# Kernel optimization log

Measured on AMD Instinct MI355X. Metric: run time of the kernel, lower is better.

Reference implementation:

```python
import jax, jax.numpy as jnp
import numpy as np

EMBED_DIM = 1024
HEAD_DIM = 64


def setup_inputs() -> dict:
    key = jax.random.key(0)
    ks = jax.random.split(key, 7)
    B, S = 4, 2048
    x = jax.random.normal(ks[0], (B, S, EMBED_DIM), dtype=jnp.float32)
    s = EMBED_DIM ** -0.5  # torch Linear default init scale (uniform bound)
    Wk = jax.random.uniform(ks[1], (EMBED_DIM, HEAD_DIM), minval=-s, maxval=s)
    bk = jax.random.uniform(ks[2], (HEAD_DIM,), minval=-s, maxval=s)
    Wq = jax.random.uniform(ks[3], (EMBED_DIM, HEAD_DIM), minval=-s, maxval=s)
    bq = jax.random.uniform(ks[4], (HEAD_DIM,), minval=-s, maxval=s)
    Wv = jax.random.uniform(ks[5], (EMBED_DIM, HEAD_DIM), minval=-s, maxval=s)
    bv = jax.random.uniform(ks[6], (HEAD_DIM,), minval=-s, maxval=s)
    return {"x": x, "Wq": Wq, "bq": bq, "Wk": Wk, "bk": bk, "Wv": Wv, "bv": bv}


def reference(x, Wq, bq, Wk, bk, Wv, bv):
    # projections: [B,S,D]
    q = x @ Wq + bq
    k = x @ Wk + bk
    v = x @ Wv + bv
    # NOTE: faithful to source, which DIVIDES by head_dim**-0.5 (i.e. multiplies by sqrt(d))
    scale = HEAD_DIM ** -0.5
    wei = jnp.einsum('bqd,bkd->bqk', q, k) / scale  # [B,S,S]
    S = x.shape[1]
    causal = jnp.tril(jnp.ones((S, S), dtype=bool))
    wei = jnp.where(causal, wei, -jnp.inf)
    attn_weights = jax.nn.softmax(wei, axis=-1)
    return jnp.einsum('bqk,bkd->bqd', attn_weights, v)
```

## Files before the change

kernel.cpp:

```cpp
#include <hip/hip_runtime.h>
#include <math.h>

#define S_LEN 2048
#define NB 4
#define EMB 1024
#define HD 64
#define NROW (NB * S_LEN)
#define NEG_BIG -3.0e38f
#define SC 11.5415603f
#define DEFER_THR 3.0f
#define KVSPLIT 4

typedef _Float16 half8 __attribute__((ext_vector_type(8)));
typedef _Float16 half4 __attribute__((ext_vector_type(4)));
typedef float f32x4 __attribute__((ext_vector_type(4)));

static __device__ __forceinline__ f32x4 mfma32(half8 a, half8 b, f32x4 c) {
    return __builtin_amdgcn_mfma_f32_16x16x32_f16(a, b, c, 0, 0, 0);
}
static __device__ __forceinline__ f32x4 mfma16(half4 a, half4 b, f32x4 c) {
    return __builtin_amdgcn_mfma_f32_16x16x16f16(a, b, c, 0, 0, 0);
}

__global__ __launch_bounds__(256) void prep_w(
    const float* __restrict__ Wq, const float* __restrict__ Wk,
    const float* __restrict__ Wv, _Float16* __restrict__ wt_frag)
{
    const int g  = blockIdx.x >> 4;
    const int kc = blockIdx.x & 15;
    const int k0 = kc * 64;
    const float* W = (g == 0) ? Wq : (g == 1) ? Wk : Wv;

    __shared__ float tile[64][68];
    const int t = threadIdx.x;
    {
        const int kk = t >> 2, cb = (t & 3) * 16;
#pragma unroll
        for (int i = 0; i < 4; i++)
            *(f32x4*)&tile[kk][cb + 4 * i] =
                *(const f32x4*)(W + (size_t)(k0 + kk) * HD + cb + 4 * i);
    }
    __syncthreads();

    const int c4 = t >> 6, l = t & 63;
    const int col = c4 * 16 + (l & 15);
    const int krow = (l >> 4) * 8;
#pragma unroll
    for (int sub = 0; sub < 2; sub++) {
        half8 hv;
#pragma unroll
        for (int e = 0; e < 8; e++)
            hv[e] = (_Float16)tile[sub * 32 + krow + e][col];
        const size_t addr = (size_t)(g * 4 + c4) * 16384 +
                            (size_t)(kc * 2 + sub) * 512 + (size_t)l * 8;
        *(half8*)(wt_frag + addr) = hv;
    }
}

__global__ __launch_bounds__(768) void proj_kernel(
    const float* __restrict__ x, const _Float16* __restrict__ wt_frag,
    const float* __restrict__ bq, const float* __restrict__ bk,
    const float* __restrict__ bv,
    _Float16* __restrict__ qs, _Float16* __restrict__ kh_,
    _Float16* __restrict__ vt)
{
    const int m0 = blockIdx.x * 32;
    const int t = threadIdx.x, lane = t & 63, w = t >> 6;

    __shared__ __align__(16) _Float16 xs[32][1032];

    for (int i = t; i < 4096; i += 768) {
        const int row = i >> 7, off = (i & 127) * 8;
        const float* xp = x + (size_t)(m0 + row) * EMB + off;
        const f32x4 v0 = *(const f32x4*)xp;
        const f32x4 v1 = *(const f32x4*)(xp + 4);
        half8 h;
#pragma unroll
        for (int jj = 0; jj < 4; jj++) {
            h[jj]     = (_Float16)v0[jj];
            h[4 + jj] = (_Float16)v1[jj];
        }
        *(half8*)&xs[row][off] = h;
    }

    const int f = w;
    const int row0 = lane & 15, kq = lane >> 4;
    const _Float16* wp = wt_frag + (size_t)f * 16384 + (size_t)lane * 8;

    half8 wbuf[4];
#pragma unroll
    for (int c = 0; c < 4; c++) wbuf[c] = *(const half8*)(wp + (size_t)c * 512);

    __syncthreads();

    f32x4 acc0 = f32x4{0, 0, 0, 0}, acc1 = f32x4{0, 0, 0, 0};

#pragma unroll
    for (int c = 0; c < 32; ++c) {
        const half8 ax0 = *(const half8*)&xs[row0][c * 32 + kq * 8];
        const half8 ax1 = *(const half8*)&xs[16 + row0][c * 32 + kq * 8];
        const half8 bw = wbuf[c & 3];
        acc0 = mfma32(ax0, bw, acc0);
        acc1 = mfma32(ax1, bw, acc1);
        if (c + 4 < 32) wbuf[c & 3] = *(const half8*)(wp + (size_t)(c + 4) * 512);
    }

    const int mat = f >> 2, c4 = f & 3;
    const int mcol = c4 * 16 + (lane & 15);
    const float bb = ((mat == 0) ? bq : (mat == 1) ? bk : bv)[mcol];
#pragma unroll
    for (int rh = 0; rh < 2; rh++) {
        const f32x4 acc = rh ? acc1 : acc0;
        const int grow0 = m0 + rh * 16 + kq * 4;
        if (mat == 0) {
#pragma unroll
            for (int r = 0; r < 4; r++)
                qs[(size_t)(grow0 + r) * HD + mcol] = (_Float16)((acc[r] + bb) * SC);
        } else if (mat == 1) {
#pragma unroll
            for (int r = 0; r < 4; r++)
                kh_[(size_t)(grow0 + r) * HD + mcol] = (_Float16)(acc[r] + bb);
        } else {
            half4 hv;
#pragma unroll
            for (int r = 0; r < 4; r++) hv[r] = (_Float16)(acc[r] + bb);
            const int bidx = grow0 >> 11, sr = grow0 & (S_LEN - 1);
            *(half4*)(vt + ((size_t)bidx * HD + mcol) * S_LEN + sr) = hv;
        }
    }
}

__global__ __launch_bounds__(512) void attn_kernel(
    const _Float16* __restrict__ qs, const _Float16* __restrict__ kh_,
    const _Float16* __restrict__ vt,
    _Float16* __restrict__ po, float* __restrict__ pm, float* __restrict__ pl)
{
    const int id = blockIdx.x;
    const int qq = id & 3;
    const int b  = (id >> 2) & 3;
    const int qt = 31 - (id >> 4);
    const int q0 = qt * 64;
    const int t = threadIdx.x, lane = t & 63, w = t >> 6;
    const int rf = w >> 1, kvh = w & 1;

    __shared__ __align__(16) unsigned char smem[37888];
    _Float16 (*klds)[64][72] = (_Float16(*)[64][72])smem;
    _Float16 (*vlds)[64][72] = (_Float16(*)[64][72])(smem + 18432);
    float (*obuf)[16][68] = (float(*)[16][68])smem;
    float* mbuf = (float*)(smem + 36864);
    float* lbuf = (float*)(smem + 36864 + 512);

    const size_t rowq = ((size_t)b * S_LEN + q0 + rf * 16 + (lane & 15)) * HD + (lane >> 4) * 8;
    const half8 bq0 = *(const half8*)(qs + rowq);
    const half8 bq1 = *(const half8*)(qs + rowq + 32);

    f32x4 o[4];
#pragma unroll
    for (int c = 0; c < 4; c++) o[c] = f32x4{0, 0, 0, 0};
    float m_r = NEG_BIG, l_r = 0.f;

    const int nt = qt + 1;
    const int lo = (nt * qq) >> 2, hi = (nt * (qq + 1)) >> 2;

    const size_t kbase = (size_t)b * S_LEN * HD;
    const size_t vbase = (size_t)b * HD * S_LEN;
    const int srow = t >> 3, scol = (t & 7) * 8;

    half8 sK, sV;
    auto gload = [&](int tl) {
        sK = *(const half8*)(kh_ + kbase + (size_t)(tl * 64 + srow) * HD + scol);
        sV = *(const half8*)(vt + vbase + (size_t)srow * S_LEN + tl * 64 + scol);
    };
    auto swrite = [&](int nb) {
        *(half8*)&klds[nb][srow][scol] = sK;
        *(half8*)&vlds[nb][srow][scol] = sV;
    };

    if (lo < hi) { gload(lo); swrite(0); }
    __syncthreads();

    int cur = 0;
    for (int tl = lo; tl < hi; ++tl) {
        if (tl + 1 < hi) gload(tl + 1);

        const int kv0 = tl * 64 + kvh * 32;
        __builtin_amdgcn_s_setprio(1);
        f32x4 s[2];
#pragma unroll
        for (int h = 0; h < 2; h++) {
            const int keyl = kvh * 32 + 16 * h + (lane & 15);
            f32x4 a = f32x4{0, 0, 0, 0};
            a = mfma32(*(const half8*)&klds[cur][keyl][(lane >> 4) * 8], bq0, a);
            a = mfma32(*(const half8*)&klds[cur][keyl][32 + (lane >> 4) * 8], bq1, a);
            s[h] = a;
        }
        __builtin_amdgcn_s_setprio(0);

        const int qrow = q0 + rf * 16 + (lane & 15);
        const int kb0  = kv0 + (lane >> 4) * 4;
        float tv[8];
#pragma unroll
        for (int h = 0; h < 2; h++)
#pragma unroll
            for (int r = 0; r < 4; r++)
                tv[h * 4 + r] = (kb0 + 16 * h + r <= qrow) ? s[h][r] : NEG_BIG;

        float mt = tv[0];
#pragma unroll
        for (int i = 1; i < 8; i++) mt = fmaxf(mt, tv[i]);
        mt = fmaxf(mt, __shfl_xor(mt, 16));
        mt = fmaxf(mt, __shfl_xor(mt, 32));

        if (!__all(mt <= m_r + DEFER_THR)) {
            const float mn = fmaxf(m_r, mt);
            const float corr = exp2f(m_r - mn);
            m_r = mn;
            l_r *= corr;
            float corrB[4];
#pragma unroll
            for (int r = 0; r < 4; r++) corrB[r] = __shfl(corr, (lane >> 4) * 4 + r);
#pragma unroll
            for (int c = 0; c < 4; c++)
#pragma unroll
                for (int r = 0; r < 4; r++) o[c][r] *= corrB[r];
        }

        float p[8], rs = 0.f;
#pragma unroll
        for (int i = 0; i < 8; i++) { p[i] = exp2f(tv[i] - m_r); rs += p[i]; }
        rs += __shfl_xor(rs, 16);
        rs += __shfl_xor(rs, 32);
        l_r += rs;

        half4 pa[2];
#pragma unroll
        for (int h = 0; h < 2; h++)
#pragma unroll
            for (int r = 0; r < 4; r++) pa[h][r] = (_Float16)p[h * 4 + r];
        __builtin_amdgcn_s_setprio(1);
#pragma unroll
        for (int c = 0; c < 4; c++) {
#pragma unroll
            for (int h = 0; h < 2; h++) {
                const half4 vf = *(const half4*)&vlds[cur][16 * c + (lane & 15)]
                                                    [kvh * 32 + 16 * h + (lane >> 4) * 4];
                o[c] = mfma16(pa[h], vf, o[c]);
            }
        }
        __builtin_amdgcn_s_setprio(0);

        if (tl + 1 < hi) swrite(cur ^ 1);
        __syncthreads();
        cur ^= 1;
    }

    if (lane < 16) { mbuf[w * 16 + lane] = m_r; lbuf[w * 16 + lane] = l_r; }
#pragma unroll
    for (int c = 0; c < 4; c++)
#pragma unroll
        for (int r = 0; r < 4; r++)
            obuf[w][(lane >> 4) * 4 + r][16 * c + (lane & 15)] = o[c][r];
    __syncthreads();

    if (t < 256) {
        const int row16 = t >> 4, cb = (t & 15) * 4;
#pragma unroll
        for (int rf2 = 0; rf2 < 4; rf2++) {
            const int w0 = rf2 * 2, w1 = w0 + 1;
            const float m0v = mbuf[w0 * 16 + row16], m1v = mbuf[w1 * 16 + row16];
            const float M = fmaxf(m0v, m1v);
            const float e0 = exp2f(m0v - M), e1 = exp2f(m1v - M);
            const float L = lbuf[w0 * 16 + row16] * e0 + lbuf[w1 * 16 + row16] * e1;
            const f32x4 o0 = *(const f32x4*)&obuf[w0][row16][cb];
            const f32x4 o1 = *(const f32x4*)&obuf[w1][row16][cb];
            half4 hv;
#pragma unroll
            for (int jj = 0; jj < 4; jj++) hv[jj] = (_Float16)(o0[jj] * e0 + o1[jj] * e1);
            const size_t idx = (size_t)(qq * NB + b) * S_LEN + q0 + rf2 * 16 + row16;
            *(half4*)(po + idx * HD + cb) = hv;
            if ((t & 15) == 0) { pm[idx] = M; pl[idx] = L; }
        }
    }
}

__global__ __launch_bounds__(256) void merge_kernel(
    const _Float16* __restrict__ po, const float* __restrict__ pm,
    const float* __restrict__ pl, float* __restrict__ out)
{
    const int b = blockIdx.y;
    const int row = blockIdx.x * 16 + (threadIdx.x >> 4);
    const int cb = (threadIdx.x & 15) * 4;

    float mv[KVSPLIT];
    float M = NEG_BIG;
#pragma unroll
    for (int qq = 0; qq < KVSPLIT; qq++) {
        mv[qq] = pm[(size_t)(qq * NB + b) * S_LEN + row];
        M = fmaxf(M, mv[qq]);
    }
    float L = 0.f;
    f32x4 acc = f32x4{0, 0, 0, 0};
#pragma unroll
    for (int qq = 0; qq < KVSPLIT; qq++) {
        const size_t idx = (size_t)(qq * NB + b) * S_LEN + row;
        const float e = exp2f(mv[qq] - M);
        L += pl[idx] * e;
        const half4 ov = *(const half4*)(po + idx * HD + cb);
#pragma unroll
        for (int jj = 0; jj < 4; jj++) acc[jj] += (float)ov[jj] * e;
    }
    const float inv = 1.0f / L;
    f32x4 res;
#pragma unroll
    for (int jj = 0; jj < 4; jj++) res[jj] = acc[jj] * inv;
    *(f32x4*)(out + ((size_t)b * S_LEN + row) * HD + cb) = res;
}

extern "C" void kernel_launch(void* const* d_in, const int* in_sizes, int n_in,
                              void* d_out, int out_size, void* d_ws, size_t ws_size,
                              hipStream_t stream) {
    const float* x  = (const float*)d_in[0];
    const float* Wq = (const float*)d_in[1];
    const float* bq = (const float*)d_in[2];
    const float* Wk = (const float*)d_in[3];
    const float* bk = (const float*)d_in[4];
    const float* Wv = (const float*)d_in[5];
    const float* bv = (const float*)d_in[6];
    float* out = (float*)d_out;

    _Float16* ws = (_Float16*)d_ws;
    const size_t nW = (size_t)192 * EMB;
    const size_t n  = (size_t)NROW * HD;
    _Float16* wt_frag = ws;
    _Float16* qsb = wt_frag + nW;
    _Float16* khb = qsb + n;
    _Float16* vtb = khb + n;
    _Float16* po = vtb + n;
    float* pm = (float*)(po + (size_t)KVSPLIT * NB * S_LEN * HD);
    float* pl = pm + (size_t)KVSPLIT * NB * S_LEN;

    prep_w<<<48, 256, 0, stream>>>(Wq, Wk, Wv, wt_frag);
    proj_kernel<<<NROW / 32, 768, 0, stream>>>(
        x, wt_frag, bq, bk, bv, qsb, khb, vtb);
    attn_kernel<<<32 * NB * KVSPLIT, 512, 0, stream>>>(qsb, khb, vtb, po, pm, pl);
    merge_kernel<<<dim3(S_LEN / 16, NB), 256, 0, stream>>>(po, pm, pl, out);
}
```

Measured before the change: 36.73 us.

## Halve projection row tile and give each wave two output column fragments

The projection kernel now processes 16 rows per block with 384 threads, and each wave computes two 16-column output fragments that share the same x fragment. This doubles the grid to 512 blocks for better CU occupancy and halves LDS use per block. The cost is that every weight fragment is reloaded by twice as many blocks. prep_w is also retiled to 96 smaller blocks, each converting a 32-row chunk of the weights.

```diff
diff --git a/kernel.cpp b/kernel.cpp
--- a/kernel.cpp
+++ b/kernel.cpp
@@ -26,50 +26,43 @@
     const float* __restrict__ Wq, const float* __restrict__ Wk,
     const float* __restrict__ Wv, _Float16* __restrict__ wt_frag)
 {
-    const int g  = blockIdx.x >> 4;
-    const int kc = blockIdx.x & 15;
-    const int k0 = kc * 64;
+    const int g   = blockIdx.x >> 5;
+    const int c32 = blockIdx.x & 31;
+    const int k0  = c32 * 32;
     const float* W = (g == 0) ? Wq : (g == 1) ? Wk : Wv;
 
-    __shared__ float tile[64][68];
+    __shared__ float tile[32][68];
     const int t = threadIdx.x;
     {
-        const int kk = t >> 2, cb = (t & 3) * 16;
-#pragma unroll
-        for (int i = 0; i < 4; i++)
-            *(f32x4*)&tile[kk][cb + 4 * i] =
-                *(const f32x4*)(W + (size_t)(k0 + kk) * HD + cb + 4 * i);
+        const int kk = t >> 3, cb = (t & 7) * 8;
+        *(f32x4*)&tile[kk][cb]     = *(const f32x4*)(W + (size_t)(k0 + kk) * HD + cb);
+        *(f32x4*)&tile[kk][cb + 4] = *(const f32x4*)(W + (size_t)(k0 + kk) * HD + cb + 4);
     }
     __syncthreads();
 
     const int c4 = t >> 6, l = t & 63;
     const int col = c4 * 16 + (l & 15);
     const int krow = (l >> 4) * 8;
-#pragma unroll
-    for (int sub = 0; sub < 2; sub++) {
-        half8 hv;
-#pragma unroll
-        for (int e = 0; e < 8; e++)
-            hv[e] = (_Float16)tile[sub * 32 + krow + e][col];
-        const size_t addr = (size_t)(g * 4 + c4) * 16384 +
-                            (size_t)(kc * 2 + sub) * 512 + (size_t)l * 8;
-        *(half8*)(wt_frag + addr) = hv;
-    }
-}
-
-__global__ __launch_bounds__(768) void proj_kernel(
+    half8 hv;
+#pragma unroll
+    for (int e = 0; e < 8; e++) hv[e] = (_Float16)tile[krow + e][col];
+    *(half8*)(wt_frag + (size_t)(g * 4 + c4) * 16384 +
+              (size_t)c32 * 512 + (size_t)l * 8) = hv;
+}
+
+__global__ __launch_bounds__(384) void proj_kernel(
     const float* __restrict__ x, const _Float16* __restrict__ wt_frag,
     const float* __restrict__ bq, const float* __restrict__ bk,
     const float* __restrict__ bv,
     _Float16* __restrict__ qs, _Float16* __restrict__ kh_,
     _Float16* __restrict__ vt)
 {
-    const int m0 = blockIdx.x * 32;
+    const int m0 = blockIdx.x * 16;
     const int t = threadIdx.x, lane = t & 63, w = t >> 6;
 
-    __shared__ __align__(16) _Float16 xs[32][1032];
-
-    for (int i = t; i < 4096; i += 768) {
+    __shared__ __align__(16) _Float16 xs[16][1032];
+
+    for (int i = t; i < 2048; i += 384) {
         const int row = i >> 7, off = (i & 127) * 8;
         const float* xp = x + (size_t)(m0 + row) * EMB + off;
         const f32x4 v0 = *(const f32x4*)xp;
@@ -83,13 +76,17 @@
         *(half8*)&xs[row][off] = h;
     }
 
-    const int f = w;
+    const int f0 = w * 2;
     const int row0 = lane & 15, kq = lane >> 4;
-    const _Float16* wp = wt_frag + (size_t)f * 16384 + (size_t)lane * 8;
-
-    half8 wbuf[4];
-#pragma unroll
-    for (int c = 0; c < 4; c++) wbuf[c] = *(const half8*)(wp + (size_t)c * 512);
+    const _Float16* wp0 = wt_frag + (size_t)f0 * 16384 + (size_t)lane * 8;
+    const _Float16* wp1 = wp0 + 16384;
+
+    half8 wbuf0[4], wbuf1[4];
+#pragma unroll
+    for (int c = 0; c < 4; c++) {
+        wbuf0[c] = *(const half8*)(wp0 + (size_t)c * 512);
+        wbuf1[c] = *(const half8*)(wp1 + (size_t)c * 512);
+    }
 
     __syncthreads();
 
@@ -97,21 +94,23 @@
 
 #pragma unroll
     for (int c = 0; c < 32; ++c) {
-        const half8 ax0 = *(const half8*)&xs[row0][c * 32 + kq * 8];
-        const half8 ax1 = *(const half8*)&xs[16 + row0][c * 32 + kq * 8];
-        const half8 bw = wbuf[c & 3];
-        acc0 = mfma32(ax0, bw, acc0);
-        acc1 = mfma32(ax1, bw, acc1);
-        if (c + 4 < 32) wbuf[c & 3] = *(const half8*)(wp + (size_t)(c + 4) * 512);
-    }
-
-    const int mat = f >> 2, c4 = f & 3;
-    const int mcol = c4 * 16 + (lane & 15);
-    const float bb = ((mat == 0) ? bq : (mat == 1) ? bk : bv)[mcol];
-#pragma unroll
-    for (int rh = 0; rh < 2; rh++) {
-        const f32x4 acc = rh ? acc1 : acc0;
-        const int grow0 = m0 + rh * 16 + kq * 4;
+        const half8 ax = *(const half8*)&xs[row0][c * 32 + kq * 8];
+        acc0 = mfma32(ax, wbuf0[c & 3], acc0);
+        acc1 = mfma32(ax, wbuf1[c & 3], acc1);
+        if (c + 4 < 32) {
+            wbuf0[c & 3] = *(const half8*)(wp0 + (size_t)(c + 4) * 512);
+            wbuf1[c & 3] = *(const half8*)(wp1 + (size_t)(c + 4) * 512);
+        }
+    }
+
+#pragma unroll
+    for (int jf = 0; jf < 2; jf++) {
+        const int f = f0 + jf;
+        const f32x4 acc = jf ? acc1 : acc0;
+        const int mat = f >> 2, c4 = f & 3;
+        const int mcol = c4 * 16 + (lane & 15);
+        const float bb = ((mat == 0) ? bq : (mat == 1) ? bk : bv)[mcol];
+        const int grow0 = m0 + kq * 4;
         if (mat == 0) {
 #pragma unroll
             for (int r = 0; r < 4; r++)
@@ -339,8 +338,8 @@
     float* pm = (float*)(po + (size_t)KVSPLIT * NB * S_LEN * HD);
     float* pl = pm + (size_t)KVSPLIT * NB * S_LEN;
 
-    prep_w<<<48, 256, 0, stream>>>(Wq, Wk, Wv, wt_frag);
-    proj_kernel<<<NROW / 32, 768, 0, stream>>>(
+    prep_w<<<96, 256, 0, stream>>>(Wq, Wk, Wv, wt_frag);
+    proj_kernel<<<NROW / 16, 384, 0, stream>>>(
         x, wt_frag, bq, bk, bv, qsb, khb, vtb);
     attn_kernel<<<32 * NB * KVSPLIT, 512, 0, stream>>>(qsb, khb, vtb, po, pm, pl);
     merge_kernel<<<dim3(S_LEN / 16, NB), 256, 0, stream>>>(po, pm, pl, out);
```

Result: slower. 40.45 us (+10.1%).
